# Performance work log

Hardware: AMD Instinct MI355X
Metric: run time of the kernel (lower is better)

Reference implementation:

```python
import jax, jax.numpy as jnp
import numpy as np

B, T, C = 4, 2048, 1024
H = 16
D = C // H  # head_dim = 64
SCALE = D ** -0.5


def setup_inputs() -> dict:
    key = jax.random.key(0)
    k1, k2, k3 = jax.random.split(key, 3)
    x = jax.random.normal(k1, (B, T, C), dtype=jnp.float32)
    w_qkv = jax.random.normal(k2, (C, 3 * C), dtype=jnp.float32) * (C ** -0.5)
    w_proj = jax.random.normal(k3, (C, C), dtype=jnp.float32) * (C ** -0.5)
    return {"x": x, "w_qkv": w_qkv, "w_proj": w_proj}


def reference(x, w_qkv, w_proj):
    Bx, Tx, Cx = x.shape
    qkv = x @ w_qkv                        # [B, T, 3C]
    q, k, v = jnp.split(qkv, 3, axis=-1)   # each [B, T, C]
    # [B, T, H, D] -> [B, H, T, D]
    q = q.reshape(Bx, Tx, H, D).transpose(0, 2, 1, 3)
    k = k.reshape(Bx, Tx, H, D).transpose(0, 2, 1, 3)
    v = v.reshape(Bx, Tx, H, D).transpose(0, 2, 1, 3)
    att = jnp.einsum('bhqd,bhkd->bhqk', q, k) * SCALE  # [B, H, T, T]
    causal = jnp.tril(jnp.ones((Tx, Tx), dtype=bool))
    att = jnp.where(causal[None, None], att, -jnp.inf)
    att = jax.nn.softmax(att, axis=-1)
    # dropout p=0.0 (eval-mode reference): identity
    y = jnp.einsum('bhqk,bhkd->bhqd', att, v)          # [B, H, T, D]
    y = y.transpose(0, 2, 1, 3).reshape(Bx, Tx, Cx)    # [B, T, C]
    return y @ w_proj
```

## Files before the change

### kernel.cpp

```cpp
#include <hip/hip_runtime.h>
#include <hip/hip_bf16.h>

#define Bdim 4
#define Tdim 2048
#define Cdim 1024
#define Hdim 16
#define Ddim 64
#define SCALE_Q 0.18033688011112042f

using f32x4  = __attribute__((ext_vector_type(4))) float;
using short8 = __attribute__((ext_vector_type(8))) short;

union U8 { uint4 v; unsigned short s[8]; };

__device__ __forceinline__ float bf2f(unsigned short u) {
  union { unsigned int i; float f; } x; x.i = ((unsigned int)u) << 16; return x.f;
}
__device__ __forceinline__ unsigned short f2bf(float f) {
  union { float f; unsigned int i; } x; x.f = f;
  unsigned int lsb = (x.i >> 16) & 1u;
  unsigned int r = x.i + 0x7fffu + lsb;
  return (unsigned short)(r >> 16);
}

__device__ __forceinline__ unsigned int pk_bf16(float lo, float hi) {
  union { __hip_bfloat162 h; unsigned int u; } c;
  c.h = __float22bfloat162_rn(make_float2(lo, hi));
  return c.u;
}

__device__ __forceinline__ float fexp2(float x) {
#if __has_builtin(__builtin_amdgcn_exp2f)
  return __builtin_amdgcn_exp2f(x);
#else
  return exp2f(x);
#endif
}

__device__ __forceinline__ void glds16(const unsigned short* g, unsigned short* l) {
  __builtin_amdgcn_global_load_lds(
      (const __attribute__((address_space(1))) void*)g,
      (__attribute__((address_space(3))) void*)l,
      16, 0, 0);
}

__device__ __forceinline__ int detect_fmt(const unsigned int* xw) {
  int cnt = 0;
  for (int i = 0; i < 64; i++) {
    unsigned int e = (xw[i] >> 7) & 0xFFu;
    if (e >= 100u && e <= 140u) cnt++;
  }
  return (cnt >= 40) ? 1 : 0;
}

__global__ void detect_kernel(const unsigned int* __restrict__ x, int* __restrict__ flag) {
  if (threadIdx.x == 0) *flag = detect_fmt(x);
}

__global__ __launch_bounds__(256) void prep_kernel(
    const void* __restrict__ x, const void* __restrict__ wq, const void* __restrict__ wp,
    unsigned short* __restrict__ X16, unsigned short* __restrict__ WqT,
    unsigned short* __restrict__ WpT, int* __restrict__ flag)
{
  __shared__ __align__(16) unsigned short Ts[64][72];
  __shared__ int sfmt;
  if (threadIdx.x == 0) {
    const int f = detect_fmt((const unsigned int*)x);
    sfmt = f;
    if (blockIdx.x == 0) *flag = f;
  }
  __syncthreads();
  const int fmt = sfmt;
  const unsigned bid = blockIdx.x;
  const int tid = threadIdx.x;

  if (bid < 4096u) {
    const size_t i = (size_t)bid * 256 + tid;
    if (fmt == 1) {
      *(uint4*)(X16 + i * 8) = *(const uint4*)((const unsigned short*)x + i * 8);
    } else {
      const float* s = (const float*)x + i * 8;
      float4 a = *(const float4*)(s);
      float4 b = *(const float4*)(s + 4);
      U8 o;
      o.s[0]=f2bf(a.x); o.s[1]=f2bf(a.y); o.s[2]=f2bf(a.z); o.s[3]=f2bf(a.w);
      o.s[4]=f2bf(b.x); o.s[5]=f2bf(b.y); o.s[6]=f2bf(b.z); o.s[7]=f2bf(b.w);
      *(uint4*)(X16 + i * 8) = o.v;
    }
    return;
  }

  const void* W; unsigned short* WT; int N, K, n0, k0;
  if (bid < 4864u) {
    const int t = bid - 4096;
    W = wq; WT = WqT; N = 3072; K = 1024;
    n0 = (t % 48) * 64; k0 = (t / 48) * 64;
  } else {
    const int t = bid - 4864;
    W = wp; WT = WpT; N = 1024; K = 1024;
    n0 = (t & 15) * 64; k0 = (t >> 4) * 64;
  }
  const int r = tid >> 2, c0 = (tid & 3) * 16;

  if (fmt == 0) {
    const float* Wf = (const float*)W + (size_t)(k0 + r) * N + n0 + c0;
    #pragma unroll
    for (int j4 = 0; j4 < 4; j4++) {
      float4 v = *(const float4*)(Wf + j4 * 4);
      Ts[r][c0 + j4*4 + 0] = f2bf(v.x);
      Ts[r][c0 + j4*4 + 1] = f2bf(v.y);
      Ts[r][c0 + j4*4 + 2] = f2bf(v.z);
      Ts[r][c0 + j4*4 + 3] = f2bf(v.w);
    }
  } else {
    const unsigned short* Wh = (const unsigned short*)W + (size_t)(k0 + r) * N + n0 + c0;
    uint4 v0 = *(const uint4*)(Wh);
    uint4 v1 = *(const uint4*)(Wh + 8);
    *(uint4*)&Ts[r][c0] = v0;
    *(uint4*)&Ts[r][c0 + 8] = v1;
  }
  __syncthreads();

  U8 o0, o1;
  #pragma unroll
  for (int j = 0; j < 8; j++) { o0.s[j] = Ts[c0 + j][r]; o1.s[j] = Ts[c0 + 8 + j][r]; }
  unsigned short* dst = WT + (size_t)(n0 + r) * K + k0 + c0;
  *(uint4*)(dst)     = o0.v;
  *(uint4*)(dst + 8) = o1.v;
}

__global__ __launch_bounds__(256) void vtrans_kernel(
    const unsigned short* __restrict__ Vb, unsigned short* __restrict__ VbT)
{
  __shared__ __align__(16) unsigned short Ts[64][72];
  const int tid = threadIdx.x;
  const int head = blockIdx.x >> 5;
  const int tt   = blockIdx.x & 31;
  const int r = tid >> 2, c0 = (tid & 3) * 16;

  const unsigned short* src = Vb + (size_t)head * Tdim * Ddim + (size_t)(tt * 64 + r) * Ddim + c0;
  uint4 a = *(const uint4*)(src);
  uint4 b = *(const uint4*)(src + 8);
  *(uint4*)&Ts[r][c0]     = a;
  *(uint4*)&Ts[r][c0 + 8] = b;
  __syncthreads();

  U8 o0, o1;
  #pragma unroll
  for (int j = 0; j < 8; j++) { o0.s[j] = Ts[c0 + j][r]; o1.s[j] = Ts[c0 + 8 + j][r]; }
  unsigned short* dst = VbT + (size_t)head * Tdim * Ddim + (size_t)r * Tdim + tt * 64 + c0;
  *(uint4*)(dst)     = o0.v;
  *(uint4*)(dst + 8) = o1.v;
}

__global__ __launch_bounds__(256) void gemm128b_kernel(
    const unsigned short* __restrict__ A16,
    const unsigned short* __restrict__ BT16,
    void* __restrict__ Cout,
    unsigned short* __restrict__ Qb,
    unsigned short* __restrict__ Kb,
    unsigned short* __restrict__ Vb,
    const int* __restrict__ flag,
    int M, int N, int K, int mode)
{
  __shared__ __align__(16) unsigned short As[2][128 * 32];
  __shared__ __align__(16) unsigned short Bs[2][128 * 32];

  const int fmt = *flag;
  const int tid  = threadIdx.x;
  const int wave = tid >> 6;
  const int lane = tid & 63;
  const int col  = lane & 15;
  const int quad = lane >> 4;
  const int m0 = blockIdx.x * 128;
  const int n0 = blockIdx.y * 128;
  const int wm = (wave >> 1) * 64;
  const int wn = (wave & 1) * 64;

  const int lr = lane >> 2;
  const int lc = (lane & 3) * 8;

  f32x4 acc[4][4];
  #pragma unroll
  for (int i = 0; i < 4; i++)
    #pragma unroll
    for (int j = 0; j < 4; j++) acc[i][j] = (f32x4){0.f, 0.f, 0.f, 0.f};

  const unsigned short* Ap0 = A16  + (size_t)(m0 + wave * 32 + lr) * K + lc;
  const unsigned short* Ap1 = A16  + (size_t)(m0 + wave * 32 + 16 + lr) * K + lc;
  const unsigned short* Bp0 = BT16 + (size_t)(n0 + wave * 32 + lr) * K + lc;
  const unsigned short* Bp1 = BT16 + (size_t)(n0 + wave * 32 + 16 + lr) * K + lc;
  unsigned short* a0 = &As[0][wave * 32 * 32];
  unsigned short* a0b = &As[0][(wave * 32 + 16) * 32];
  unsigned short* a1 = &As[1][wave * 32 * 32];
  unsigned short* a1b = &As[1][(wave * 32 + 16) * 32];
  unsigned short* b0 = &Bs[0][wave * 32 * 32];
  unsigned short* b0b = &Bs[0][(wave * 32 + 16) * 32];
  unsigned short* b1 = &Bs[1][wave * 32 * 32];
  unsigned short* b1b = &Bs[1][(wave * 32 + 16) * 32];

  for (int k0 = 0; k0 < K; k0 += 64) {
    glds16(Ap0,      a0);  glds16(Ap0 + 32, a1);
    glds16(Ap1,      a0b); glds16(Ap1 + 32, a1b);
    glds16(Bp0,      b0);  glds16(Bp0 + 32, b1);
    glds16(Bp1,      b0b); glds16(Bp1 + 32, b1b);
    Ap0 += 64; Ap1 += 64; Bp0 += 64; Bp1 += 64;
    __syncthreads();

    #pragma unroll
    for (int half = 0; half < 2; half++) {
      short8 afr[4], bfr[4];
      #pragma unroll
      for (int mi = 0; mi < 4; mi++)
        afr[mi] = *(const short8*)&As[half][(wm + mi * 16 + col) * 32 + quad * 8];
      #pragma unroll
      for (int ni = 0; ni < 4; ni++)
        bfr[ni] = *(const short8*)&Bs[half][(wn + ni * 16 + col) * 32 + quad * 8];
      #pragma unroll
      for (int mi = 0; mi < 4; mi++)
        #pragma unroll
        for (int ni = 0; ni < 4; ni++)
          acc[mi][ni] = __builtin_amdgcn_mfma_f32_16x16x32_bf16(afr[mi], bfr[ni], acc[mi][ni], 0, 0, 0);
    }
    __syncthreads();
  }

  if (mode == 1) {
    const int bb = m0 >> 11;
    const int tBase = (m0 & 2047) + wm;
    #pragma unroll
    for (int ni = 0; ni < 4; ni++) {
      const int n = n0 + wn + ni * 16 + col;
      const int which = n >> 10;
      const int rem = n & 1023;
      const int h = rem >> 6;
      const int d = rem & 63;
      unsigned short* dstBase = (which == 0) ? Qb : (which == 1 ? Kb : Vb);
      const float scale = (which == 0) ? SCALE_Q : 1.f;
      dstBase += (size_t)(bb * Hdim + h) * Tdim * Ddim + d;
      #pragma unroll
      for (int mi = 0; mi < 4; mi++)
        #pragma unroll
        for (int i = 0; i < 4; i++) {
          const int t = tBase + mi * 16 + quad * 4 + i;
          dstBase[(size_t)t * Ddim] = f2bf(acc[mi][ni][i] * scale);
        }
    }
  } else {
    #pragma unroll
    for (int mi = 0; mi < 4; mi++)
      #pragma unroll
      for (int ni = 0; ni < 4; ni++)
        #pragma unroll
        for (int i = 0; i < 4; i++) {
          const int m = m0 + wm + mi * 16 + quad * 4 + i;
          const int n = n0 + wn + ni * 16 + col;
          const float v = acc[mi][ni][i];
          if (fmt == 0) ((float*)Cout)[(size_t)m * N + n] = v;
          else ((unsigned short*)Cout)[(size_t)m * N + n] = f2bf(v);
        }
  }
}

#define XBM 128
#define XBN 128
#define XBK 32
#define XLDK 40

__global__ __launch_bounds__(256) void gemm128_kernel(
    const unsigned short* __restrict__ A16,
    const void* __restrict__ Bsrc,
    void* __restrict__ Cout,
    unsigned short* __restrict__ Qb,
    unsigned short* __restrict__ Kb,
    unsigned short* __restrict__ Vb,
    const int* __restrict__ flag,
    int M, int N, int K, int mode, int bFmt)
{
  __shared__ __align__(16) unsigned short As[XBM * XLDK];
  __shared__ __align__(16) unsigned short Bs[XBN * XLDK];

  const int fmt = *flag;
  const int tid  = threadIdx.x;
  const int wave = tid >> 6;
  const int lane = tid & 63;
  const int col  = lane & 15;
  const int quad = lane >> 4;
  const int m0 = blockIdx.x * XBM;
  const int n0 = blockIdx.y * XBN;
  const int wm = (wave >> 1) * 64;
  const int wn = (wave & 1) * 64;

  const int ar = tid >> 1;
  const int ah = (tid & 1) * 16;

  f32x4 acc[4][4];
  #pragma unroll
  for (int i = 0; i < 4; i++)
    #pragma unroll
    for (int j = 0; j < 4; j++) acc[i][j] = (f32x4){0.f, 0.f, 0.f, 0.f};

  for (int k0 = 0; k0 < K; k0 += XBK) {
    {
      const unsigned short* Ap = A16 + (size_t)(m0 + ar) * K + k0 + ah;
      uint4 a0 = *(const uint4*)(Ap);
      uint4 a1 = *(const uint4*)(Ap + 8);
      *(uint4*)&As[ar * XLDK + ah]     = a0;
      *(uint4*)&As[ar * XLDK + ah + 8] = a1;
    }
    if (bFmt == 1) {
      const unsigned short* Bp = (const unsigned short*)Bsrc + (size_t)(n0 + ar) * K + k0 + ah;
      uint4 b0 = *(const uint4*)(Bp);
      uint4 b1 = *(const uint4*)(Bp + 8);
      *(uint4*)&Bs[ar * XLDK + ah]     = b0;
      *(uint4*)&Bs[ar * XLDK + ah + 8] = b1;
    } else {
      const int bn = tid & 127;
      const int bg = (tid >> 7) * 16;
      U8 p0, p1;
      if (fmt == 0) {
        const float* Bf = (const float*)Bsrc;
        #pragma unroll
        for (int j = 0; j < 8; j++) {
          p0.s[j] = f2bf(Bf[(size_t)(k0 + bg + j) * N + n0 + bn]);
          p1.s[j] = f2bf(Bf[(size_t)(k0 + bg + 8 + j) * N + n0 + bn]);
        }
      } else {
        const unsigned short* Bh = (const unsigned short*)Bsrc;
        #pragma unroll
        for (int j = 0; j < 8; j++) {
          p0.s[j] = Bh[(size_t)(k0 + bg + j) * N + n0 + bn];
          p1.s[j] = Bh[(size_t)(k0 + bg + 8 + j) * N + n0 + bn];
        }
      }
      *(uint4*)&Bs[bn * XLDK + bg]     = p0.v;
      *(uint4*)&Bs[bn * XLDK + bg + 8] = p1.v;
    }
    __syncthreads();

    short8 afr[4], bfr[4];
    #pragma unroll
    for (int mi = 0; mi < 4; mi++)
      afr[mi] = *(const short8*)&As[(wm + mi * 16 + col) * XLDK + quad * 8];
    #pragma unroll
    for (int ni = 0; ni < 4; ni++)
      bfr[ni] = *(const short8*)&Bs[(wn + ni * 16 + col) * XLDK + quad * 8];
    #pragma unroll
    for (int mi = 0; mi < 4; mi++)
      #pragma unroll
      for (int ni = 0; ni < 4; ni++)
        acc[mi][ni] = __builtin_amdgcn_mfma_f32_16x16x32_bf16(afr[mi], bfr[ni], acc[mi][ni], 0, 0, 0);
    __syncthreads();
  }

  #pragma unroll
  for (int mi = 0; mi < 4; mi++) {
    #pragma unroll
    for (int ni = 0; ni < 4; ni++) {
      #pragma unroll
      for (int i = 0; i < 4; i++) {
        const int m = m0 + wm + mi * 16 + quad * 4 + i;
        const int n = n0 + wn + ni * 16 + col;
        const float v = acc[mi][ni][i];
        if (mode == 0) {
          if (fmt == 0) ((float*)Cout)[(size_t)m * N + n] = v;
          else ((unsigned short*)Cout)[(size_t)m * N + n] = f2bf(v);
        } else {
          const int which = n >> 10;
          const int rem = n & 1023;
          const int h = rem >> 6;
          const int d = rem & 63;
          const int b = m >> 11;
          const int t = m & 2047;
          const size_t idx = ((size_t)(b * Hdim + h) * Tdim + t) * Ddim + d;
          if      (which == 0) Qb[idx] = f2bf(v * SCALE_Q);
          else if (which == 1) Kb[idx] = f2bf(v);
          else                 Vb[idx] = f2bf(v);
        }
      }
    }
  }
}

#define BM 64
#define BN 64
#define BK 32
#define LDK 40

__global__ __launch_bounds__(256) void gemm64_kernel(
    const void* __restrict__ A,
    const void* __restrict__ Bw,
    void* __restrict__ Cout,
    unsigned short* __restrict__ Qb,
    unsigned short* __restrict__ Kb,
    unsigned short* __restrict__ Vb,
    const int* __restrict__ flag,
    int M, int N, int K, int mode, int aFmt, int outFmt, int aOff, int mOff)
{
  __shared__ __align__(16) unsigned short As[BM * LDK];
  __shared__ __align__(16) unsigned short Bs[BN * LDK];

  const int fmt = *flag;
  const int af  = (aFmt  == 2) ? fmt : aFmt;
  const int of  = (outFmt == 2) ? fmt : outFmt;

  const int tid  = threadIdx.x;
  const int wave = tid >> 6;
  const int lane = tid & 63;
  const int m0 = blockIdx.x * BM;
  const int n0 = blockIdx.y * BN;

  const int ar = tid >> 2;
  const int ak = (tid & 3) * 8;
  const int bk = tid >> 3;
  const int bn = (tid & 7) * 8;

  const int lr = lane & 15;
  const int lq = lane >> 4;

  f32x4 acc[4] = {{0,0,0,0},{0,0,0,0},{0,0,0,0},{0,0,0,0}};

  for (int k0 = 0; k0 < K; k0 += BK) {
    U8 a8;
    if (af == 1) {
      a8.v = *(const uint4*)((const unsigned short*)A + (size_t)(aOff + m0 + ar) * K + (k0 + ak));
    } else {
      const float* Af = (const float*)A + (size_t)(aOff + m0 + ar) * K + (k0 + ak);
      float4 x0 = *(const float4*)(Af);
      float4 x1 = *(const float4*)(Af + 4);
      a8.s[0] = f2bf(x0.x); a8.s[1] = f2bf(x0.y); a8.s[2] = f2bf(x0.z); a8.s[3] = f2bf(x0.w);
      a8.s[4] = f2bf(x1.x); a8.s[5] = f2bf(x1.y); a8.s[6] = f2bf(x1.z); a8.s[7] = f2bf(x1.w);
    }
    *(uint4*)(&As[ar * LDK + ak]) = a8.v;

    U8 b8;
    if (fmt == 1) {
      b8.v = *(const uint4*)((const unsigned short*)Bw + (size_t)(k0 + bk) * N + (n0 + bn));
    } else {
      const float* Bf = (const float*)Bw + (size_t)(k0 + bk) * N + (n0 + bn);
      float4 x0 = *(const float4*)(Bf);
      float4 x1 = *(const float4*)(Bf + 4);
      b8.s[0] = f2bf(x0.x); b8.s[1] = f2bf(x0.y); b8.s[2] = f2bf(x0.z); b8.s[3] = f2bf(x0.w);
      b8.s[4] = f2bf(x1.x); b8.s[5] = f2bf(x1.y); b8.s[6] = f2bf(x1.z); b8.s[7] = f2bf(x1.w);
    }
    #pragma unroll
    for (int i = 0; i < 8; i++) Bs[(bn + i) * LDK + bk] = b8.s[i];
    __syncthreads();

    short8 afrag = *(const short8*)(&As[(wave * 16 + lr) * LDK + lq * 8]);
    #pragma unroll
    for (int c = 0; c < 4; c++) {
      short8 bfrag = *(const short8*)(&Bs[(c * 16 + lr) * LDK + lq * 8]);
      acc[c] = __builtin_amdgcn_mfma_f32_16x16x32_bf16(afrag, bfrag, acc[c], 0, 0, 0);
    }
    __syncthreads();
  }

  #pragma unroll
  for (int c = 0; c < 4; c++) {
    #pragma unroll
    for (int i = 0; i < 4; i++) {
      const int m = m0 + wave * 16 + lq * 4 + i;
      const int n = n0 + c * 16 + lr;
      const float v = acc[c][i];
      if (mode == 0) {
        if (of == 0) ((float*)Cout)[(size_t)(mOff + m) * N + n] = v;
        else ((unsigned short*)Cout)[(size_t)(mOff + m) * N + n] = f2bf(v);
      } else {
        const int which = n >> 10;
        const int rem = n & 1023;
        const int h = rem >> 6;
        const int d = rem & 63;
        const int b = m >> 11;
        const int t = m & 2047;
        const size_t idx = ((size_t)(b * Hdim + h) * Tdim + t) * Ddim + d;
        if      (which == 0) Qb[idx] = f2bf(v * SCALE_Q);
        else if (which == 1) Kb[idx] = f2bf(v);
        else                 Vb[idx] = f2bf(v);
      }
    }
  }
}

__global__ __launch_bounds__(256) void attn128_kernel(
    const unsigned short* __restrict__ Qb,
    const unsigned short* __restrict__ Kb,
    const unsigned short* __restrict__ Vb,
    const unsigned short* __restrict__ VbT,
    unsigned short* __restrict__ Y)
{
  __shared__ __align__(16) unsigned short Ks[64 * 72];
  __shared__ __align__(16) unsigned short Vt[64 * 72];
  __shared__ __align__(16) unsigned short Pw[4][32 * 72];

  const int tid  = threadIdx.x;
  const int wave = tid >> 6;
  const int lane = tid & 63;
  const int col  = lane & 15;
  const int quad = lane >> 4;

  const int pair = blockIdx.x & 7;
  const int bh   = blockIdx.x >> 3;
  const size_t headOff = (size_t)bh * Tdim * Ddim;

  const int sr = tid >> 2;
  const int sc = (tid & 3) * 16;

  const int b = bh >> 4;
  const int h = bh & 15;

  const short8 onesf = {16256, 16256, 16256, 16256, 16256, 16256, 16256, 16256};

  #pragma unroll
  for (int half = 0; half < 2; half++) {
    const int qt = half ? (15 - pair) : pair;
    const int qb = qt * 128;
    const int nkt = (qb >> 6) + 2;
    const int rMin = qb + wave * 32;
    const int rMax = rMin + 31;

    short8 qf[2][2];
    #pragma unroll
    for (int mi = 0; mi < 2; mi++) {
      const unsigned short* Qr = Qb + headOff + (size_t)(rMin + mi * 16 + col) * Ddim;
      qf[mi][0] = *(const short8*)(Qr + quad * 8);
      qf[mi][1] = *(const short8*)(Qr + 32 + quad * 8);
    }

    f32x4 o_acc[2][4];
    f32x4 l_acc[2];
    #pragma unroll
    for (int mi = 0; mi < 2; mi++) {
      l_acc[mi] = (f32x4){0.f, 0.f, 0.f, 0.f};
      #pragma unroll
      for (int n = 0; n < 4; n++) o_acc[mi][n] = (f32x4){0.f, 0.f, 0.f, 0.f};
    }

    uint4 kr0, kr1, vr0, vr1;
    {
      const unsigned short* Kr = Kb + headOff + (size_t)sr * Ddim + sc;
      kr0 = *(const uint4*)(Kr);
      kr1 = *(const uint4*)(Kr + 8);
      if (VbT) {
        const unsigned short* Vr = VbT + headOff + (size_t)sr * Tdim + sc;
        vr0 = *(const uint4*)(Vr);
        vr1 = *(const uint4*)(Vr + 8);
      } else {
        const unsigned short* Vr = Vb + headOff + (size_t)sr * Ddim + sc;
        vr0 = *(const uint4*)(Vr);
        vr1 = *(const uint4*)(Vr + 8);
      }
    }

    for (int kt = 0; kt < nkt; kt++) {
      __syncthreads();
      *(uint4*)&Ks[sr * 72 + sc]     = kr0;
      *(uint4*)&Ks[sr * 72 + sc + 8] = kr1;
      if (VbT) {
        *(uint4*)&Vt[sr * 72 + sc]     = vr0;
        *(uint4*)&Vt[sr * 72 + sc + 8] = vr1;
      } else {
        U8 v0, v1; v0.v = vr0; v1.v = vr1;
        #pragma unroll
        for (int j = 0; j < 8; j++) {
          Vt[(sc + j) * 72 + sr]     = v0.s[j];
          Vt[(sc + 8 + j) * 72 + sr] = v1.s[j];
        }
      }
      __syncthreads();

      if (kt + 1 < nkt) {
        const int kb = (kt + 1) * 64;
        const unsigned short* Kr = Kb + headOff + (size_t)(kb + sr) * Ddim + sc;
        kr0 = *(const uint4*)(Kr);
        kr1 = *(const uint4*)(Kr + 8);
        if (VbT) {
          const unsigned short* Vr = VbT + headOff + (size_t)sr * Tdim + kb + sc;
          vr0 = *(const uint4*)(Vr);
          vr1 = *(const uint4*)(Vr + 8);
        } else {
          const unsigned short* Vr = Vb + headOff + (size_t)(kb + sr) * Ddim + sc;
          vr0 = *(const uint4*)(Vr);
          vr1 = *(const uint4*)(Vr + 8);
        }
      }

      const int ktb = kt * 64;
      if (ktb <= rMax) {
        f32x4 s_acc[4][2];
        #pragma unroll
        for (int c = 0; c < 4; c++) {
          const unsigned short* Kl = &Ks[(c * 16 + col) * 72];
          short8 kf0 = *(const short8*)(Kl + quad * 8);
          short8 kf1 = *(const short8*)(Kl + 32 + quad * 8);
          #pragma unroll
          for (int mi = 0; mi < 2; mi++) {
            f32x4 z = {0.f, 0.f, 0.f, 0.f};
            z = __builtin_amdgcn_mfma_f32_16x16x32_bf16(kf0, qf[mi][0], z, 0, 0, 0);
            s_acc[c][mi] = __builtin_amdgcn_mfma_f32_16x16x32_bf16(kf1, qf[mi][1], z, 0, 0, 0);
          }
        }

        if (ktb + 63 > rMin) {
          #pragma unroll
          for (int c = 0; c < 4; c++)
            #pragma unroll
            for (int mi = 0; mi < 2; mi++)
              #pragma unroll
              for (int i = 0; i < 4; i++)
                if (ktb + c * 16 + quad * 4 + i > rMin + mi * 16 + col)
                  s_acc[c][mi][i] = -1e30f;
        }

        #pragma unroll
        for (int mi = 0; mi < 2; mi++)
          #pragma unroll
          for (int c = 0; c < 4; c++) {
            const float p0 = fexp2(fminf(s_acc[c][mi][0], 80.f));
            const float p1 = fexp2(fminf(s_acc[c][mi][1], 80.f));
            const float p2 = fexp2(fminf(s_acc[c][mi][2], 80.f));
            const float p3 = fexp2(fminf(s_acc[c][mi][3], 80.f));
            const unsigned int u0 = pk_bf16(p0, p1);
            const unsigned int u1 = pk_bf16(p2, p3);
            uint2* dst = (uint2*)&Pw[wave][(mi * 16 + col) * 72 + c * 16 + quad * 4];
            *dst = make_uint2(u0, u1);
          }

        short8 pf[2][2];
        #pragma unroll
        for (int mi = 0; mi < 2; mi++) {
          pf[mi][0] = *(const short8*)(&Pw[wave][(mi * 16 + col) * 72 + quad * 8]);
          pf[mi][1] = *(const short8*)(&Pw[wave][(mi * 16 + col) * 72 + 32 + quad * 8]);
          l_acc[mi] = __builtin_amdgcn_mfma_f32_16x16x32_bf16(pf[mi][0], onesf, l_acc[mi], 0, 0, 0);
          l_acc[mi] = __builtin_amdgcn_mfma_f32_16x16x32_bf16(pf[mi][1], onesf, l_acc[mi], 0, 0, 0);
        }
        #pragma unroll
        for (int n = 0; n < 4; n++) {
          const unsigned short* Vl = &Vt[(n * 16 + col) * 72];
          short8 vf0 = *(const short8*)(Vl + quad * 8);
          short8 vf1 = *(const short8*)(Vl + 32 + quad * 8);
          #pragma unroll
          for (int mi = 0; mi < 2; mi++) {
            o_acc[mi][n] = __builtin_amdgcn_mfma_f32_16x16x32_bf16(pf[mi][0], vf0, o_acc[mi][n], 0, 0, 0);
            o_acc[mi][n] = __builtin_amdgcn_mfma_f32_16x16x32_bf16(pf[mi][1], vf1, o_acc[mi][n], 0, 0, 0);
          }
        }
      }
    }

    #pragma unroll
    for (int mi = 0; mi < 2; mi++)
      #pragma unroll
      for (int i = 0; i < 4; i++) {
        const float inv = 1.f / l_acc[mi][i];
        const int qrow = rMin + mi * 16 + quad * 4 + i;
        unsigned short* dst = Y + (size_t)(b * Tdim + qrow) * Cdim + h * Ddim;
        #pragma unroll
        for (int n = 0; n < 4; n++)
          dst[n * 16 + col] = f2bf(o_acc[mi][n][i] * inv);
      }
  }
}

extern "C" void kernel_launch(void* const* d_in, const int* in_sizes, int n_in,
                              void* d_out, int out_size, void* d_ws, size_t ws_size,
                              hipStream_t stream) {
  const void* x      = d_in[0];
  const void* w_qkv  = d_in[1];
  const void* w_proj = d_in[2];

  int* flag = (int*)d_ws;
  unsigned short* wsb = (unsigned short*)((char*)d_ws + 1024);

  const size_t HS = (size_t)Bdim * Hdim * Tdim * Ddim;
  const size_t FULL  = 1024 + 2 * (4 * HS + (size_t)3072 * 1024 + (size_t)1024 * 1024);
  const size_t FULL2 = FULL + 2 * HS;
  const size_t MONO  = 1024 + 2 * (4 * HS);

  dim3 blk(256);

  if (ws_size >= FULL) {
    unsigned short* Qb  = wsb;
    unsigned short* Kb  = Qb + HS;
    unsigned short* Vb  = Kb + HS;
    unsigned short* XY  = Vb + HS;
    unsigned short* WqT = XY + HS;
    unsigned short* WpT = WqT + (size_t)3072 * 1024;
    unsigned short* VbT = WpT + (size_t)1024 * 1024;
    const int M = Bdim * Tdim;

    prep_kernel<<<dim3(5120), blk, 0, stream>>>(x, w_qkv, w_proj, XY, WqT, WpT, flag);

    gemm128b_kernel<<<dim3(M / 128, 3072 / 128), blk, 0, stream>>>(
        XY, WqT, nullptr, Qb, Kb, Vb, flag, M, 3072, Cdim, 1);

    if (ws_size >= FULL2) {
      vtrans_kernel<<<dim3(Bdim * Hdim * (Tdim / 64)), blk, 0, stream>>>(Vb, VbT);
      attn128_kernel<<<dim3(Bdim * Hdim * 8), blk, 0, stream>>>(Qb, Kb, Vb, VbT, XY);
    } else {
      attn128_kernel<<<dim3(Bdim * Hdim * 8), blk, 0, stream>>>(Qb, Kb, Vb, nullptr, XY);
    }

    gemm128b_kernel<<<dim3(M / 128, Cdim / 128), blk, 0, stream>>>(
        XY, WpT, d_out, nullptr, nullptr, nullptr, flag, M, Cdim, Cdim, 0);
  } else if (ws_size >= MONO) {
    detect_kernel<<<1, 64, 0, stream>>>((const unsigned int*)x, flag);
    const size_t HSb = (size_t)Hdim * Tdim * Ddim;
    unsigned short* Qb2 = wsb;
    unsigned short* Kb2 = Qb2 + HSb;
    unsigned short* Vb2 = Kb2 + HSb;
    unsigned short* Y2  = Vb2 + HSb;
    for (int b = 0; b < Bdim; b++) {
      gemm64_kernel<<<dim3(Tdim / BM, 3072 / BN), blk, 0, stream>>>(
          x, w_qkv, nullptr, Qb2, Kb2, Vb2, flag,
          Tdim, 3072, Cdim, 1, 2, 2, b * Tdim, 0);
      attn128_kernel<<<dim3(Hdim * 8), blk, 0, stream>>>(Qb2, Kb2, Vb2, nullptr, Y2);
      gemm64_kernel<<<dim3(Tdim / BM, Cdim / BN), blk, 0, stream>>>(
          Y2, w_proj, d_out, nullptr, nullptr, nullptr, flag,
          Tdim, Cdim, Cdim, 0, 1, 2, 0, b * Tdim);
    }
  } else {
    detect_kernel<<<1, 64, 0, stream>>>((const unsigned int*)x, flag);
    const size_t HSb = (size_t)Hdim * Tdim * Ddim;
    unsigned short* Qb = wsb;
    unsigned short* Kb = Qb + HSb;
    unsigned short* Vb = Kb + HSb;
    unsigned short* Y2 = Vb + HSb;

    for (int b = 0; b < Bdim; b++) {
      gemm64_kernel<<<dim3(Tdim / BM, 3072 / BN), blk, 0, stream>>>(
          x, w_qkv, nullptr, Qb, Kb, Vb, flag,
          Tdim, 3072, Cdim, 1, 2, 2, b * Tdim, 0);

      attn128_kernel<<<dim3(Hdim * 8), blk, 0, stream>>>(Qb, Kb, Vb, nullptr, Y2);

      gemm64_kernel<<<dim3(Tdim / BM, Cdim / BN), blk, 0, stream>>>(
          Y2, w_proj, d_out, nullptr, nullptr, nullptr, flag,
          Tdim, Cdim, Cdim, 0, 1, 2, 0, b * Tdim);
    }
  }
}
```

Baseline: 259.6 us.

## Fuse V transpose into QKV GEMM epilogue, swizzle LDS, double-buffer, set MFMA priority

```diff
diff --git a/kernel.cpp b/kernel.cpp
--- a/kernel.cpp
+++ b/kernel.cpp
@@ -13,9 +13,6 @@
 
 union U8 { uint4 v; unsigned short s[8]; };
 
-__device__ __forceinline__ float bf2f(unsigned short u) {
-  union { unsigned int i; float f; } x; x.i = ((unsigned int)u) << 16; return x.f;
-}
 __device__ __forceinline__ unsigned short f2bf(float f) {
   union { float f; unsigned int i; } x; x.f = f;
   unsigned int lsb = (x.i >> 16) & 1u;
@@ -129,31 +126,7 @@
   *(uint4*)(dst + 8) = o1.v;
 }
 
-__global__ __launch_bounds__(256) void vtrans_kernel(
-    const unsigned short* __restrict__ Vb, unsigned short* __restrict__ VbT)
-{
-  __shared__ __align__(16) unsigned short Ts[64][72];
-  const int tid = threadIdx.x;
-  const int head = blockIdx.x >> 5;
-  const int tt   = blockIdx.x & 31;
-  const int r = tid >> 2, c0 = (tid & 3) * 16;
-
-  const unsigned short* src = Vb + (size_t)head * Tdim * Ddim + (size_t)(tt * 64 + r) * Ddim + c0;
-  uint4 a = *(const uint4*)(src);
-  uint4 b = *(const uint4*)(src + 8);
-  *(uint4*)&Ts[r][c0]     = a;
-  *(uint4*)&Ts[r][c0 + 8] = b;
-  __syncthreads();
-
-  U8 o0, o1;
-  #pragma unroll
-  for (int j = 0; j < 8; j++) { o0.s[j] = Ts[c0 + j][r]; o1.s[j] = Ts[c0 + 8 + j][r]; }
-  unsigned short* dst = VbT + (size_t)head * Tdim * Ddim + (size_t)r * Tdim + tt * 64 + c0;
-  *(uint4*)(dst)     = o0.v;
-  *(uint4*)(dst + 8) = o1.v;
-}
-
-__global__ __launch_bounds__(256) void gemm128b_kernel(
+__global__ __launch_bounds__(256) void gemm128c_kernel(
     const unsigned short* __restrict__ A16,
     const unsigned short* __restrict__ BT16,
     void* __restrict__ Cout,
@@ -161,7 +134,7 @@
     unsigned short* __restrict__ Kb,
     unsigned short* __restrict__ Vb,
     const int* __restrict__ flag,
-    int M, int N, int K, int mode)
+    int M, int N, int K, int mode, int vT)
 {
   __shared__ __align__(16) unsigned short As[2][128 * 32];
   __shared__ __align__(16) unsigned short Bs[2][128 * 32];
@@ -177,8 +150,9 @@
   const int wm = (wave >> 1) * 64;
   const int wn = (wave & 1) * 64;
 
-  const int lr = lane >> 2;
-  const int lc = (lane & 3) * 8;
+  const int r4 = lane >> 2;
+  const int schunk = ((lane & 3) ^ ((lane >> 3) & 3)) * 8;
+  const int rsw = (quad ^ ((col >> 1) & 3)) * 8;
 
   f32x4 acc[4][4];
   #pragma unroll
@@ -186,44 +160,45 @@
     #pragma unroll
     for (int j = 0; j < 4; j++) acc[i][j] = (f32x4){0.f, 0.f, 0.f, 0.f};
 
-  const unsigned short* Ap0 = A16  + (size_t)(m0 + wave * 32 + lr) * K + lc;
-  const unsigned short* Ap1 = A16  + (size_t)(m0 + wave * 32 + 16 + lr) * K + lc;
-  const unsigned short* Bp0 = BT16 + (size_t)(n0 + wave * 32 + lr) * K + lc;
-  const unsigned short* Bp1 = BT16 + (size_t)(n0 + wave * 32 + 16 + lr) * K + lc;
-  unsigned short* a0 = &As[0][wave * 32 * 32];
-  unsigned short* a0b = &As[0][(wave * 32 + 16) * 32];
-  unsigned short* a1 = &As[1][wave * 32 * 32];
-  unsigned short* a1b = &As[1][(wave * 32 + 16) * 32];
-  unsigned short* b0 = &Bs[0][wave * 32 * 32];
-  unsigned short* b0b = &Bs[0][(wave * 32 + 16) * 32];
-  unsigned short* b1 = &Bs[1][wave * 32 * 32];
-  unsigned short* b1b = &Bs[1][(wave * 32 + 16) * 32];
-
-  for (int k0 = 0; k0 < K; k0 += 64) {
-    glds16(Ap0,      a0);  glds16(Ap0 + 32, a1);
-    glds16(Ap1,      a0b); glds16(Ap1 + 32, a1b);
-    glds16(Bp0,      b0);  glds16(Bp0 + 32, b1);
-    glds16(Bp1,      b0b); glds16(Bp1 + 32, b1b);
-    Ap0 += 64; Ap1 += 64; Bp0 += 64; Bp1 += 64;
+  const unsigned short* ApA = A16  + (size_t)(m0 + wave * 32 + r4) * K + schunk;
+  const unsigned short* ApB = ApA + (size_t)16 * K;
+  const unsigned short* BpA = BT16 + (size_t)(n0 + wave * 32 + r4) * K + schunk;
+  const unsigned short* BpB = BpA + (size_t)16 * K;
+
+#define STAGE(BUF, KS) do { \
+    glds16(ApA + (KS) * 32, &As[BUF][wave * 32 * 32]);        \
+    glds16(ApB + (KS) * 32, &As[BUF][(wave * 32 + 16) * 32]); \
+    glds16(BpA + (KS) * 32, &Bs[BUF][wave * 32 * 32]);        \
+    glds16(BpB + (KS) * 32, &Bs[BUF][(wave * 32 + 16) * 32]); \
+  } while (0)
+
+#define COMPUTE(BUF) do { \
+    short8 afr[4], bfr[4]; \
+    _Pragma("unroll") \
+    for (int mi = 0; mi < 4; mi++) \
+      afr[mi] = *(const short8*)&As[BUF][(wm + mi * 16 + col) * 32 + rsw]; \
+    _Pragma("unroll") \
+    for (int ni = 0; ni < 4; ni++) \
+      bfr[ni] = *(const short8*)&Bs[BUF][(wn + ni * 16 + col) * 32 + rsw]; \
+    _Pragma("unroll") \
+    for (int mi = 0; mi < 4; mi++) \
+      _Pragma("unroll") \
+      for (int ni = 0; ni < 4; ni++) \
+        acc[mi][ni] = __builtin_amdgcn_mfma_f32_16x16x32_bf16(afr[mi], bfr[ni], acc[mi][ni], 0, 0, 0); \
+  } while (0)
+
+  const int NK = K >> 5;
+  STAGE(0, 0);
+  for (int ks = 0; ks < NK; ks += 2) {
     __syncthreads();
-
-    #pragma unroll
-    for (int half = 0; half < 2; half++) {
-      short8 afr[4], bfr[4];
-      #pragma unroll
-      for (int mi = 0; mi < 4; mi++)
-        afr[mi] = *(const short8*)&As[half][(wm + mi * 16 + col) * 32 + quad * 8];
-      #pragma unroll
-      for (int ni = 0; ni < 4; ni++)
-        bfr[ni] = *(const short8*)&Bs[half][(wn + ni * 16 + col) * 32 + quad * 8];
-      #pragma unroll
-      for (int mi = 0; mi < 4; mi++)
-        #pragma unroll
-        for (int ni = 0; ni < 4; ni++)
-          acc[mi][ni] = __builtin_amdgcn_mfma_f32_16x16x32_bf16(afr[mi], bfr[ni], acc[mi][ni], 0, 0, 0);
-    }
+    if (ks + 1 < NK) STAGE(1, ks + 1);
+    COMPUTE(0);
     __syncthreads();
-  }
+    if (ks + 2 < NK) STAGE(0, ks + 2);
+    COMPUTE(1);
+  }
+#undef STAGE
+#undef COMPUTE
 
   if (mode == 1) {
     const int bb = m0 >> 11;
@@ -235,16 +210,27 @@
       const int rem = n & 1023;
       const int h = rem >> 6;
       const int d = rem & 63;
-      unsigned short* dstBase = (which == 0) ? Qb : (which == 1 ? Kb : Vb);
-      const float scale = (which == 0) ? SCALE_Q : 1.f;
-      dstBase += (size_t)(bb * Hdim + h) * Tdim * Ddim + d;
-      #pragma unroll
-      for (int mi = 0; mi < 4; mi++)
-        #pragma unroll
-        for (int i = 0; i < 4; i++) {
-          const int t = tBase + mi * 16 + quad * 4 + i;
-          dstBase[(size_t)t * Ddim] = f2bf(acc[mi][ni][i] * scale);
-        }
+      if (which == 2 && vT) {
+        unsigned short* base = Vb + (size_t)(bb * Hdim + h) * Tdim * Ddim
+                                  + (size_t)d * Tdim + tBase;
+        #pragma unroll
+        for (int mi = 0; mi < 4; mi++) {
+          const int t0 = mi * 16 + quad * 4;
+          *(uint2*)(base + t0) = make_uint2(pk_bf16(acc[mi][ni][0], acc[mi][ni][1]),
+                                            pk_bf16(acc[mi][ni][2], acc[mi][ni][3]));
+        }
+      } else {
+        unsigned short* dstBase = (which == 0) ? Qb : (which == 1 ? Kb : Vb);
+        const float scale = (which == 0) ? SCALE_Q : 1.f;
+        dstBase += (size_t)(bb * Hdim + h) * Tdim * Ddim + d;
+        #pragma unroll
+        for (int mi = 0; mi < 4; mi++)
+          #pragma unroll
+          for (int i = 0; i < 4; i++) {
+            const int t = tBase + mi * 16 + quad * 4 + i;
+            dstBase[(size_t)t * Ddim] = f2bf(acc[mi][ni][i] * scale);
+          }
+      }
     }
   } else {
     #pragma unroll
@@ -259,126 +245,6 @@
           if (fmt == 0) ((float*)Cout)[(size_t)m * N + n] = v;
           else ((unsigned short*)Cout)[(size_t)m * N + n] = f2bf(v);
         }
-  }
-}
-
-#define XBM 128
-#define XBN 128
-#define XBK 32
-#define XLDK 40
-
-__global__ __launch_bounds__(256) void gemm128_kernel(
-    const unsigned short* __restrict__ A16,
-    const void* __restrict__ Bsrc,
-    void* __restrict__ Cout,
-    unsigned short* __restrict__ Qb,
-    unsigned short* __restrict__ Kb,
-    unsigned short* __restrict__ Vb,
-    const int* __restrict__ flag,
-    int M, int N, int K, int mode, int bFmt)
-{
-  __shared__ __align__(16) unsigned short As[XBM * XLDK];
-  __shared__ __align__(16) unsigned short Bs[XBN * XLDK];
-
-  const int fmt = *flag;
-  const int tid  = threadIdx.x;
-  const int wave = tid >> 6;
-  const int lane = tid & 63;
-  const int col  = lane & 15;
-  const int quad = lane >> 4;
-  const int m0 = blockIdx.x * XBM;
-  const int n0 = blockIdx.y * XBN;
-  const int wm = (wave >> 1) * 64;
-  const int wn = (wave & 1) * 64;
-
-  const int ar = tid >> 1;
-  const int ah = (tid & 1) * 16;
-
-  f32x4 acc[4][4];
-  #pragma unroll
-  for (int i = 0; i < 4; i++)
-    #pragma unroll
-    for (int j = 0; j < 4; j++) acc[i][j] = (f32x4){0.f, 0.f, 0.f, 0.f};
-
-  for (int k0 = 0; k0 < K; k0 += XBK) {
-    {
-      const unsigned short* Ap = A16 + (size_t)(m0 + ar) * K + k0 + ah;
-      uint4 a0 = *(const uint4*)(Ap);
-      uint4 a1 = *(const uint4*)(Ap + 8);
-      *(uint4*)&As[ar * XLDK + ah]     = a0;
-      *(uint4*)&As[ar * XLDK + ah + 8] = a1;
-    }
-    if (bFmt == 1) {
-      const unsigned short* Bp = (const unsigned short*)Bsrc + (size_t)(n0 + ar) * K + k0 + ah;
-      uint4 b0 = *(const uint4*)(Bp);
-      uint4 b1 = *(const uint4*)(Bp + 8);
-      *(uint4*)&Bs[ar * XLDK + ah]     = b0;
-      *(uint4*)&Bs[ar * XLDK + ah + 8] = b1;
-    } else {
-      const int bn = tid & 127;
-      const int bg = (tid >> 7) * 16;
-      U8 p0, p1;
-      if (fmt == 0) {
-        const float* Bf = (const float*)Bsrc;
-        #pragma unroll
-        for (int j = 0; j < 8; j++) {
-          p0.s[j] = f2bf(Bf[(size_t)(k0 + bg + j) * N + n0 + bn]);
-          p1.s[j] = f2bf(Bf[(size_t)(k0 + bg + 8 + j) * N + n0 + bn]);
-        }
-      } else {
-        const unsigned short* Bh = (const unsigned short*)Bsrc;
-        #pragma unroll
-        for (int j = 0; j < 8; j++) {
-          p0.s[j] = Bh[(size_t)(k0 + bg + j) * N + n0 + bn];
-          p1.s[j] = Bh[(size_t)(k0 + bg + 8 + j) * N + n0 + bn];
-        }
-      }
-      *(uint4*)&Bs[bn * XLDK + bg]     = p0.v;
-      *(uint4*)&Bs[bn * XLDK + bg + 8] = p1.v;
-    }
-    __syncthreads();
-
-    short8 afr[4], bfr[4];
-    #pragma unroll
-    for (int mi = 0; mi < 4; mi++)
-      afr[mi] = *(const short8*)&As[(wm + mi * 16 + col) * XLDK + quad * 8];
-    #pragma unroll
-    for (int ni = 0; ni < 4; ni++)
-      bfr[ni] = *(const short8*)&Bs[(wn + ni * 16 + col) * XLDK + quad * 8];
-    #pragma unroll
-    for (int mi = 0; mi < 4; mi++)
-      #pragma unroll
-      for (int ni = 0; ni < 4; ni++)
-        acc[mi][ni] = __builtin_amdgcn_mfma_f32_16x16x32_bf16(afr[mi], bfr[ni], acc[mi][ni], 0, 0, 0);
-    __syncthreads();
-  }
-
-  #pragma unroll
-  for (int mi = 0; mi < 4; mi++) {
-    #pragma unroll
-    for (int ni = 0; ni < 4; ni++) {
-      #pragma unroll
-      for (int i = 0; i < 4; i++) {
-        const int m = m0 + wm + mi * 16 + quad * 4 + i;
-        const int n = n0 + wn + ni * 16 + col;
-        const float v = acc[mi][ni][i];
-        if (mode == 0) {
-          if (fmt == 0) ((float*)Cout)[(size_t)m * N + n] = v;
-          else ((unsigned short*)Cout)[(size_t)m * N + n] = f2bf(v);
-        } else {
-          const int which = n >> 10;
-          const int rem = n & 1023;
-          const int h = rem >> 6;
-          const int d = rem & 63;
-          const int b = m >> 11;
-          const int t = m & 2047;
-          const size_t idx = ((size_t)(b * Hdim + h) * Tdim + t) * Ddim + d;
-          if      (which == 0) Qb[idx] = f2bf(v * SCALE_Q);
-          else if (which == 1) Kb[idx] = f2bf(v);
-          else                 Vb[idx] = f2bf(v);
-        }
-      }
-    }
   }
 }
 
@@ -588,6 +454,7 @@
       const int ktb = kt * 64;
       if (ktb <= rMax) {
         f32x4 s_acc[4][2];
+        __builtin_amdgcn_s_setprio(1);
         #pragma unroll
         for (int c = 0; c < 4; c++) {
           const unsigned short* Kl = &Ks[(c * 16 + col) * 72];
@@ -600,6 +467,7 @@
             s_acc[c][mi] = __builtin_amdgcn_mfma_f32_16x16x32_bf16(kf1, qf[mi][1], z, 0, 0, 0);
           }
         }
+        __builtin_amdgcn_s_setprio(0);
 
         if (ktb + 63 > rMin) {
           #pragma unroll
@@ -627,6 +495,7 @@
           }
 
         short8 pf[2][2];
+        __builtin_amdgcn_s_setprio(1);
         #pragma unroll
         for (int mi = 0; mi < 2; mi++) {
           pf[mi][0] = *(const short8*)(&Pw[wave][(mi * 16 + col) * 72 + quad * 8]);
@@ -645,6 +514,7 @@
             o_acc[mi][n] = __builtin_amdgcn_mfma_f32_16x16x32_bf16(pf[mi][1], vf1, o_acc[mi][n], 0, 0, 0);
           }
         }
+        __builtin_amdgcn_s_setprio(0);
       }
     }
 
@@ -691,18 +561,18 @@
 
     prep_kernel<<<dim3(5120), blk, 0, stream>>>(x, w_qkv, w_proj, XY, WqT, WpT, flag);
 
-    gemm128b_kernel<<<dim3(M / 128, 3072 / 128), blk, 0, stream>>>(
-        XY, WqT, nullptr, Qb, Kb, Vb, flag, M, 3072, Cdim, 1);
-
     if (ws_size >= FULL2) {
-      vtrans_kernel<<<dim3(Bdim * Hdim * (Tdim / 64)), blk, 0, stream>>>(Vb, VbT);
-      attn128_kernel<<<dim3(Bdim * Hdim * 8), blk, 0, stream>>>(Qb, Kb, Vb, VbT, XY);
+      gemm128c_kernel<<<dim3(M / 128, 3072 / 128), blk, 0, stream>>>(
+          XY, WqT, nullptr, Qb, Kb, VbT, flag, M, 3072, Cdim, 1, 1);
+      attn128_kernel<<<dim3(Bdim * Hdim * 8), blk, 0, stream>>>(Qb, Kb, nullptr, VbT, XY);
     } else {
+      gemm128c_kernel<<<dim3(M / 128, 3072 / 128), blk, 0, stream>>>(
+          XY, WqT, nullptr, Qb, Kb, Vb, flag, M, 3072, Cdim, 1, 0);
       attn128_kernel<<<dim3(Bdim * Hdim * 8), blk, 0, stream>>>(Qb, Kb, Vb, nullptr, XY);
     }
 
-    gemm128b_kernel<<<dim3(M / 128, Cdim / 128), blk, 0, stream>>>(
-        XY, WpT, d_out, nullptr, nullptr, nullptr, flag, M, Cdim, Cdim, 0);
+    gemm128c_kernel<<<dim3(M / 128, Cdim / 128), blk, 0, stream>>>(
+        XY, WpT, d_out, nullptr, nullptr, nullptr, flag, M, Cdim, Cdim, 0, 0);
   } else if (ws_size >= MONO) {
     detect_kernel<<<1, 64, 0, stream>>>((const unsigned int*)x, flag);
     const size_t HSb = (size_t)Hdim * Tdim * Ddim;
```

Measured after the change: 261.6 us. About the same (+0.8%).
